# Kernel tuning notes

Measured on AMD Instinct MI355X. Metric: run time of the kernel, lower is better.

Reference implementation:

```python
import jax, jax.numpy as jnp
import numpy as np

B, TQ, TP, D = 4, 512, 512, 256


def setup_inputs() -> dict:
    key = jax.random.key(0)
    ks = jax.random.split(key, 5)
    return {
        "q": jax.random.normal(ks[0], (B, TQ, D), dtype=jnp.float32),
        "p": jax.random.normal(ks[1], (B, TP, D), dtype=jnp.float32),
        "W0": jax.random.normal(ks[2], (D, D), dtype=jnp.float32) / np.sqrt(D),
        "W1": jax.random.normal(ks[3], (D, D), dtype=jnp.float32) / np.sqrt(D),
        "vc": jax.random.normal(ks[4], (D, 1), dtype=jnp.float32) * 0.05,
    }


def reference(q, p, W0, W1, vc):
    # q: [B,Tq,Dq], p: [B,Tp,Dp]
    prod_q = jnp.einsum('bqd,de->bqe', q, W0)   # [B,Tq,dim]
    prod_p = jnp.einsum('bpd,de->bpe', p, W1)   # [B,Tp,dim]
    # additive attention energies: tanh over broadcast sum [B,Tp,Tq,dim]
    energy = jnp.tanh(prod_p[:, :, None, :] + prod_q[:, None, :, :])
    scores = jnp.einsum('bpqe,e->bpq', energy, vc[:, 0])  # [B,Tp,Tq]
    # original softmax is over axis=-2 of [B,Tp,Tq], i.e. the Tp axis
    weights = jax.nn.softmax(scores, axis=1)   # [B,Tp,Tq]
    # weighted sum over the Tq axis of (tiled) q
    attention_q = jnp.einsum('bpq,bqd->bpd', weights, q)  # [B,Tp,Dq]
    return attention_q
```

## Files before the change

kernel.cpp:

```cpp
#include <hip/hip_runtime.h>

#define NB 4
#define TT 512
#define DD 256
#define K2L2E    2.885390081777927f
#define NEG2L2E (-2.885390081777927f)

#if defined(__has_builtin)
# if __has_builtin(__builtin_amdgcn_global_load_lds)
#  define HAS_GLL 1
# endif
#endif

typedef float v2f __attribute__((ext_vector_type(2)));

__device__ __forceinline__ v2f pk_fma(v2f a, v2f b, v2f c) {
#if defined(__has_builtin)
# if __has_builtin(__builtin_elementwise_fma)
    return __builtin_elementwise_fma(a, b, c);
# else
    v2f r; r.x = __builtin_fmaf(a.x, b.x, c.x); r.y = __builtin_fmaf(a.y, b.y, c.y); return r;
# endif
#else
    v2f r; r.x = __builtin_fmaf(a.x, b.x, c.x); r.y = __builtin_fmaf(a.y, b.y, c.y); return r;
#endif
}
__device__ __forceinline__ v2f splat2(float s) { v2f r; r.x = s; r.y = s; return r; }

__device__ __forceinline__ void stage16(const float* __restrict__ g, float* l) {
#ifdef HAS_GLL
    __builtin_amdgcn_global_load_lds((const __attribute__((address_space(1))) void*)g,
                                     (__attribute__((address_space(3))) void*)l, 16, 0, 0);
#else
    *(float4*)l = *(const float4*)g;
#endif
}

__global__ __launch_bounds__(256) void proj_exp_kernel(
    const float* __restrict__ qin, const float* __restrict__ pin,
    const float* __restrict__ W0, const float* __restrict__ W1,
    float* __restrict__ expQ, float* __restrict__ expP)
{
    const int blk = blockIdx.x;
    const int wh = blk >> 8, tid = blk & 255;
    const int m0 = (tid >> 2) * 32, n0 = (tid & 3) * 64;
    const float* A = wh ? pin : qin;
    const float* W = wh ? W1 : W0;

    __shared__ __align__(16) float As[32 * 34];
    __shared__ __align__(16) float Bs[32 * 64];

    const int t  = threadIdx.x;
    const int ar = t >> 3, ac4 = (t & 7) * 4;
    const int br = t >> 4, bc4 = (t & 15) * 4;
    const int tm = wh ? (t >> 4) : (t & 15);
    const int tn = wh ? (t & 15) : (t >> 4);

    const float* Ap = A + (long)(m0 + ar) * DD + ac4;

    float4 av  = *(const float4*)Ap;
    float4 bv0 = *(const float4*)(W + (long)br * DD + n0 + bc4);
    float4 bv1 = *(const float4*)(W + (long)(br + 16) * DD + n0 + bc4);

    v2f accv[2][2];
    accv[0][0] = splat2(0.f); accv[0][1] = splat2(0.f);
    accv[1][0] = splat2(0.f); accv[1][1] = splat2(0.f);

    for (int c = 0; c < 8; ++c) {
        As[(ac4 + 0) * 34 + ar] = av.x;
        As[(ac4 + 1) * 34 + ar] = av.y;
        As[(ac4 + 2) * 34 + ar] = av.z;
        As[(ac4 + 3) * 34 + ar] = av.w;
        *(float4*)&Bs[br * 64 + bc4]        = bv0;
        *(float4*)&Bs[(br + 16) * 64 + bc4] = bv1;
        __syncthreads();
        if (c < 7) {
            int k1 = (c + 1) * 32;
            av  = *(const float4*)(Ap + k1);
            bv0 = *(const float4*)(W + (long)(k1 + br) * DD + n0 + bc4);
            bv1 = *(const float4*)(W + (long)(k1 + 16 + br) * DD + n0 + bc4);
        }
        #pragma unroll
        for (int kk = 0; kk < 32; ++kk) {
            float2 a = *(const float2*)&As[kk * 34 + 2 * tm];
            float4 b = *(const float4*)&Bs[kk * 64 + 4 * tn];
            v2f b01; b01.x = b.x; b01.y = b.y;
            v2f b23; b23.x = b.z; b23.y = b.w;
            accv[0][0] = pk_fma(splat2(a.x), b01, accv[0][0]);
            accv[0][1] = pk_fma(splat2(a.x), b23, accv[0][1]);
            accv[1][0] = pk_fma(splat2(a.y), b01, accv[1][0]);
            accv[1][1] = pk_fma(splat2(a.y), b23, accv[1][1]);
        }
        __syncthreads();
    }

    float acc[2][4];
    #pragma unroll
    for (int i = 0; i < 2; ++i) {
        acc[i][0] = accv[i][0].x; acc[i][1] = accv[i][0].y;
        acc[i][2] = accv[i][1].x; acc[i][3] = accv[i][1].y;
    }

    const int bi = m0 >> 9;
    const int ml = m0 & 511;
    if (wh) {
        #pragma unroll
        for (int i = 0; i < 2; ++i) {
            float4 st;
            st.x = __builtin_amdgcn_exp2f(acc[i][0] * K2L2E);
            st.y = __builtin_amdgcn_exp2f(acc[i][1] * K2L2E);
            st.z = __builtin_amdgcn_exp2f(acc[i][2] * K2L2E);
            st.w = __builtin_amdgcn_exp2f(acc[i][3] * K2L2E);
            *(float4*)(expP + ((long)bi * TT + ml + 2 * tm + i) * DD + n0 + 4 * tn) = st;
        }
    } else {
        #pragma unroll
        for (int j = 0; j < 4; ++j) {
            int d = n0 + 4 * tn + j;
            float2 st;
            st.x = __builtin_amdgcn_exp2f(acc[0][j] * K2L2E);
            st.y = __builtin_amdgcn_exp2f(acc[1][j] * K2L2E);
            *(float2*)(expQ + ((long)bi * DD + d) * TT + ml + 2 * tm) = st;
        }
    }
}

__global__ __launch_bounds__(512) void score_kernel(
    const float* __restrict__ expP, const float* __restrict__ expQ,
    const float* __restrict__ vc, float* __restrict__ ebuf, float* __restrict__ lpart)
{
    const int b = blockIdx.z, pt = blockIdx.y, qt = blockIdx.x;
    const int p0 = pt * 64, q0 = qt * 64;
    const int t  = threadIdx.x;
    const int h  = t >> 8;
    const int u  = t & 255;
    const int qx = u & 15;
    const int py = u >> 4;
    const int sw = py & 7;

    __shared__ __align__(16) float PA[64 * 256];
    __shared__ __align__(16) float QB[256 * 64];
    __shared__ __align__(16) float vcs[DD];

    const float* gP = expP + ((long)b * TT + p0) * DD;
    const float* gQ = expQ + (long)b * DD * TT + q0;

    #pragma unroll
    for (int s = 0; s < 8; ++s) {
        int f = t + 512 * s;
        int pr = f >> 6, j = f & 63;
        stage16(gP + (long)pr * DD + 4 * (j ^ ((pr >> 2) & 7)), &PA[f * 4]);
    }
    #pragma unroll
    for (int s = 0; s < 8; ++s) {
        int f = t + 512 * s;
        int d = f >> 4, o4 = (f & 15) * 4;
        stage16(gQ + (long)d * TT + o4, &QB[f * 4]);
    }
    if (t < DD) vcs[t] = vc[t];
    __syncthreads();

    v2f acc[4][2];
    #pragma unroll
    for (int i = 0; i < 4; ++i) { acc[i][0] = splat2(0.f); acc[i][1] = splat2(0.f); }
    const v2f one = splat2(1.0f);
    const float* vcb = &vcs[h * 128];

    #pragma unroll 4
    for (int dq = 0; dq < 32; ++dq) {
        const int dj = h * 32 + dq;
        float4 vq = *(const float4*)&vcb[4 * dq];
        const int sq = 4 * (dj ^ sw);
        float4 A0 = *(const float4*)&PA[(4 * py + 0) * 256 + sq];
        float4 A1 = *(const float4*)&PA[(4 * py + 1) * 256 + sq];
        float4 A2 = *(const float4*)&PA[(4 * py + 2) * 256 + sq];
        float4 A3 = *(const float4*)&PA[(4 * py + 3) * 256 + sq];
        const int db = (4 * dj) * 64 + 4 * qx;
        float4 B0 = *(const float4*)&QB[db];
        float4 B1 = *(const float4*)&QB[db + 64];
        float4 B2 = *(const float4*)&QB[db + 128];
        float4 B3 = *(const float4*)&QB[db + 192];
        v2f b0l; b0l.x = B0.x; b0l.y = B0.y;  v2f b0h; b0h.x = B0.z; b0h.y = B0.w;
        v2f b1l; b1l.x = B1.x; b1l.y = B1.y;  v2f b1h; b1h.x = B1.z; b1h.y = B1.w;
        v2f b2l; b2l.x = B2.x; b2l.y = B2.y;  v2f b2h; b2h.x = B2.z; b2h.y = B2.w;
        v2f b3l; b3l.x = B3.x; b3l.y = B3.y;  v2f b3h; b3h.x = B3.z; b3h.y = B3.w;
        #pragma unroll
        for (int i = 0; i < 4; ++i) {
            float4 a = (i == 0) ? A0 : (i == 1) ? A1 : (i == 2) ? A2 : A3;
            {
                v2f f0 = pk_fma(splat2(a.x), b0l, one);
                v2f f1 = pk_fma(splat2(a.y), b1l, one);
                v2f f2 = pk_fma(splat2(a.z), b2l, one);
                v2f f3 = pk_fma(splat2(a.w), b3l, one);
                v2f t01 = f0 * f1;
                v2f t23 = f2 * f3;
                v2f den = t01 * t23;
                v2f n01 = pk_fma(splat2(vq.x), f1, splat2(vq.y) * f0);
                v2f n23 = pk_fma(splat2(vq.z), f3, splat2(vq.w) * f2);
                v2f num = pk_fma(n01, t23, n23 * t01);
                v2f r;
                r.x = __builtin_amdgcn_rcpf(den.x);
                r.y = __builtin_amdgcn_rcpf(den.y);
                acc[i][0] = pk_fma(num, r, acc[i][0]);
            }
            {
                v2f f0 = pk_fma(splat2(a.x), b0h, one);
                v2f f1 = pk_fma(splat2(a.y), b1h, one);
                v2f f2 = pk_fma(splat2(a.z), b2h, one);
                v2f f3 = pk_fma(splat2(a.w), b3h, one);
                v2f t01 = f0 * f1;
                v2f t23 = f2 * f3;
                v2f den = t01 * t23;
                v2f n01 = pk_fma(splat2(vq.x), f1, splat2(vq.y) * f0);
                v2f n23 = pk_fma(splat2(vq.z), f3, splat2(vq.w) * f2);
                v2f num = pk_fma(n01, t23, n23 * t01);
                v2f r;
                r.x = __builtin_amdgcn_rcpf(den.x);
                r.y = __builtin_amdgcn_rcpf(den.y);
                acc[i][1] = pk_fma(num, r, acc[i][1]);
            }
        }
    }

    __syncthreads();
    float* scr = &PA[0];
    if (h == 1) {
        #pragma unroll
        for (int i = 0; i < 4; ++i) {
            float4 st;
            st.x = acc[i][0].x; st.y = acc[i][0].y;
            st.z = acc[i][1].x; st.w = acc[i][1].y;
            *(float4*)&scr[(4 * py + i) * 64 + 4 * qx] = st;
        }
    }
    __syncthreads();
    float* scr2 = &QB[0];
    if (h == 0) {
        float* eb = ebuf + ((long)b * TT + p0) * TT + q0;
        float4 colp; colp.x = 0.f; colp.y = 0.f; colp.z = 0.f; colp.w = 0.f;
        #pragma unroll
        for (int i = 0; i < 4; ++i) {
            float4 o = *(const float4*)&scr[(4 * py + i) * 64 + 4 * qx];
            float4 ev;
            ev.x = __builtin_amdgcn_exp2f((acc[i][0].x + o.x) * NEG2L2E);
            ev.y = __builtin_amdgcn_exp2f((acc[i][0].y + o.y) * NEG2L2E);
            ev.z = __builtin_amdgcn_exp2f((acc[i][1].x + o.z) * NEG2L2E);
            ev.w = __builtin_amdgcn_exp2f((acc[i][1].y + o.w) * NEG2L2E);
            *(float4*)(eb + (long)(4 * py + i) * TT + 4 * qx) = ev;
            colp.x += ev.x; colp.y += ev.y; colp.z += ev.z; colp.w += ev.w;
        }
        *(float4*)&scr2[py * 64 + 4 * qx] = colp;
    }
    __syncthreads();
    if (t < 64) {
        float s = 0.f;
        #pragma unroll
        for (int r = 0; r < 16; ++r) s += scr2[r * 64 + t];
        lpart[((long)b * 8 + pt) * TT + q0 + t] = s;
    }
}

__global__ __launch_bounds__(256) void out_kernel(
    const float* __restrict__ ebuf, const float* __restrict__ qin,
    const float* __restrict__ lpart, float* __restrict__ out)
{
    const int b = blockIdx.z, pt = blockIdx.y, dt = blockIdx.x;
    const int m0 = pt * 32, n0 = dt * 32;
    const int t    = threadIdx.x;
    const int wv   = t >> 6;
    const int lane = t & 63;
    const int pg   = lane >> 3;
    const int dg   = lane & 7;

    __shared__ __align__(16) float smem[4 * 32 * 36];
    __shared__ float linv[TT];
    float* As = smem;
    float* Bs = smem + 64 * 36;

    #pragma unroll
    for (int s = 0; s < 2; ++s) {
        int qq = t + 256 * s;
        float sum = 0.f;
        #pragma unroll
        for (int pb = 0; pb < 8; ++pb) sum += lpart[((long)b * 8 + pb) * TT + qq];
        linv[qq] = __builtin_amdgcn_rcpf(sum);
    }
    __syncthreads();

    const float* Ab = ebuf + ((long)b * TT + m0) * TT;
    const float* Bb = qin + (long)b * TT * DD + n0;

    const int ar = t >> 3, ak4 = (t & 7) * 4;

    v2f acc[4][2];
    #pragma unroll
    for (int i = 0; i < 4; ++i) { acc[i][0] = splat2(0.f); acc[i][1] = splat2(0.f); }

    for (int c = 0; c < 8; ++c) {
        const int k0 = c * 64;
        #pragma unroll
        for (int s = 0; s < 2; ++s) {
            int f = t + 256 * s, kr = f >> 3, d4 = (f & 7) * 4;
            stage16(Bb + (long)(k0 + kr) * DD + d4, &Bs[f * 4]);
        }
        #pragma unroll
        for (int s = 0; s < 2; ++s) {
            int kq = ak4 + 32 * s;
            float4 a = *(const float4*)(Ab + (long)ar * TT + k0 + kq);
            float4 lv = *(const float4*)&linv[k0 + kq];
            As[(kq + 0) * 36 + ar] = a.x * lv.x;
            As[(kq + 1) * 36 + ar] = a.y * lv.y;
            As[(kq + 2) * 36 + ar] = a.z * lv.z;
            As[(kq + 3) * 36 + ar] = a.w * lv.w;
        }
        __syncthreads();
        const int kb = 16 * wv;
        #pragma unroll
        for (int u = 0; u < 16; ++u) {
            int kk = kb + u;
            float4 a  = *(const float4*)&As[kk * 36 + 4 * pg];
            float4 bq = *(const float4*)&Bs[kk * 32 + 4 * dg];
            v2f b0; b0.x = bq.x; b0.y = bq.y;
            v2f b1; b1.x = bq.z; b1.y = bq.w;
            acc[0][0] = pk_fma(splat2(a.x), b0, acc[0][0]);
            acc[0][1] = pk_fma(splat2(a.x), b1, acc[0][1]);
            acc[1][0] = pk_fma(splat2(a.y), b0, acc[1][0]);
            acc[1][1] = pk_fma(splat2(a.y), b1, acc[1][1]);
            acc[2][0] = pk_fma(splat2(a.z), b0, acc[2][0]);
            acc[2][1] = pk_fma(splat2(a.z), b1, acc[2][1]);
            acc[3][0] = pk_fma(splat2(a.w), b0, acc[3][0]);
            acc[3][1] = pk_fma(splat2(a.w), b1, acc[3][1]);
        }
        __syncthreads();
    }

    float* scr = smem;
    #pragma unroll
    for (int i = 0; i < 4; ++i) {
        *(v2f*)&scr[wv * 1152 + (4 * pg + i) * 36 + 4 * dg]     = acc[i][0];
        *(v2f*)&scr[wv * 1152 + (4 * pg + i) * 36 + 4 * dg + 2] = acc[i][1];
    }
    __syncthreads();
    {
        int pr = t >> 3, d0 = (t & 7) * 4;
        float4 s0 = *(const float4*)&scr[0 * 1152 + pr * 36 + d0];
        float4 s1 = *(const float4*)&scr[1 * 1152 + pr * 36 + d0];
        float4 s2 = *(const float4*)&scr[2 * 1152 + pr * 36 + d0];
        float4 s3 = *(const float4*)&scr[3 * 1152 + pr * 36 + d0];
        float4 v;
        v.x = (s0.x + s1.x) + (s2.x + s3.x);
        v.y = (s0.y + s1.y) + (s2.y + s3.y);
        v.z = (s0.z + s1.z) + (s2.z + s3.z);
        v.w = (s0.w + s1.w) + (s2.w + s3.w);
        *(float4*)(out + ((long)b * TT + m0 + pr) * DD + n0 + d0) = v;
    }
}

extern "C" void kernel_launch(void* const* d_in, const int* in_sizes, int n_in,
                              void* d_out, int out_size, void* d_ws, size_t ws_size,
                              hipStream_t stream) {
    const float* q  = (const float*)d_in[0];
    const float* p  = (const float*)d_in[1];
    const float* W0 = (const float*)d_in[2];
    const float* W1 = (const float*)d_in[3];
    const float* vc = (const float*)d_in[4];
    float* out = (float*)d_out;

    float* ws    = (float*)d_ws;
    float* expQ  = ws;
    float* expP  = ws + 524288;
    float* ebuf  = ws + 1048576;
    float* lpart = ws + 2097152;

    proj_exp_kernel<<<dim3(512), 256, 0, stream>>>(q, p, W0, W1, expQ, expP);
    score_kernel<<<dim3(8, 8, NB), 512, 0, stream>>>(expP, expQ, vc, ebuf, lpart);
    out_kernel<<<dim3(8, 16, NB), 256, 0, stream>>>(ebuf, q, lpart, out);
}
```

Measured before the change: 117.2 us.

## Double-buffer LDS tiles in output GEMM kernel with register prefetch

Splits the output kernel's shared-memory tiles into two buffers. The next k-chunk of the normalized weight matrix and of q is staged while the current chunk is being multiplied, and the A-operand global loads are prefetched two chunks ahead into registers. This drops one barrier per iteration and hides global-load latency behind the FMA loop. The cost is more LDS per block, which may lower occupancy, plus higher register pressure. The kernel also relies on the epilogue scratch fitting exactly inside the doubled A buffer.

```diff
diff --git a/kernel.cpp b/kernel.cpp
--- a/kernel.cpp
+++ b/kernel.cpp
@@ -272,10 +272,9 @@
     const int pg   = lane >> 3;
     const int dg   = lane & 7;
 
-    __shared__ __align__(16) float smem[4 * 32 * 36];
+    __shared__ __align__(16) float As[2][64 * 36];
+    __shared__ __align__(16) float Bs[2][64 * 32];
     __shared__ float linv[TT];
-    float* As = smem;
-    float* Bs = smem + 64 * 36;
 
     #pragma unroll
     for (int s = 0; s < 2; ++s) {
@@ -291,35 +290,63 @@
     const float* Bb = qin + (long)b * TT * DD + n0;
 
     const int ar = t >> 3, ak4 = (t & 7) * 4;
+    const float* Arow = Ab + (long)ar * TT;
+    const int bkr = t >> 3, bd4 = (t & 7) * 4;
+
+    stage16(Bb + (long)bkr * DD + bd4,        &Bs[0][t * 4]);
+    stage16(Bb + (long)(bkr + 32) * DD + bd4, &Bs[0][1024 + t * 4]);
+    float4 av0 = *(const float4*)(Arow + ak4);
+    float4 av1 = *(const float4*)(Arow + ak4 + 32);
+    {
+        float4 l0 = *(const float4*)&linv[ak4];
+        float4 l1 = *(const float4*)&linv[ak4 + 32];
+        As[0][(ak4 + 0) * 36 + ar] = av0.x * l0.x;
+        As[0][(ak4 + 1) * 36 + ar] = av0.y * l0.y;
+        As[0][(ak4 + 2) * 36 + ar] = av0.z * l0.z;
+        As[0][(ak4 + 3) * 36 + ar] = av0.w * l0.w;
+        As[0][(ak4 + 32) * 36 + ar] = av1.x * l1.x;
+        As[0][(ak4 + 33) * 36 + ar] = av1.y * l1.y;
+        As[0][(ak4 + 34) * 36 + ar] = av1.z * l1.z;
+        As[0][(ak4 + 35) * 36 + ar] = av1.w * l1.w;
+    }
+    av0 = *(const float4*)(Arow + 64 + ak4);
+    av1 = *(const float4*)(Arow + 64 + ak4 + 32);
+    __syncthreads();
 
     v2f acc[4][2];
     #pragma unroll
     for (int i = 0; i < 4; ++i) { acc[i][0] = splat2(0.f); acc[i][1] = splat2(0.f); }
 
+    int buf = 0;
     for (int c = 0; c < 8; ++c) {
-        const int k0 = c * 64;
-        #pragma unroll
-        for (int s = 0; s < 2; ++s) {
-            int f = t + 256 * s, kr = f >> 3, d4 = (f & 7) * 4;
-            stage16(Bb + (long)(k0 + kr) * DD + d4, &Bs[f * 4]);
-        }
-        #pragma unroll
-        for (int s = 0; s < 2; ++s) {
-            int kq = ak4 + 32 * s;
-            float4 a = *(const float4*)(Ab + (long)ar * TT + k0 + kq);
-            float4 lv = *(const float4*)&linv[k0 + kq];
-            As[(kq + 0) * 36 + ar] = a.x * lv.x;
-            As[(kq + 1) * 36 + ar] = a.y * lv.y;
-            As[(kq + 2) * 36 + ar] = a.z * lv.z;
-            As[(kq + 3) * 36 + ar] = a.w * lv.w;
-        }
-        __syncthreads();
+        if (c < 7) {
+            const int k1 = (c + 1) * 64;
+            stage16(Bb + (long)(k1 + bkr) * DD + bd4,      &Bs[buf ^ 1][t * 4]);
+            stage16(Bb + (long)(k1 + 32 + bkr) * DD + bd4, &Bs[buf ^ 1][1024 + t * 4]);
+            float4 l0 = *(const float4*)&linv[k1 + ak4];
+            float4 l1 = *(const float4*)&linv[k1 + ak4 + 32];
+            As[buf ^ 1][(ak4 + 0) * 36 + ar] = av0.x * l0.x;
+            As[buf ^ 1][(ak4 + 1) * 36 + ar] = av0.y * l0.y;
+            As[buf ^ 1][(ak4 + 2) * 36 + ar] = av0.z * l0.z;
+            As[buf ^ 1][(ak4 + 3) * 36 + ar] = av0.w * l0.w;
+            As[buf ^ 1][(ak4 + 32) * 36 + ar] = av1.x * l1.x;
+            As[buf ^ 1][(ak4 + 33) * 36 + ar] = av1.y * l1.y;
+            As[buf ^ 1][(ak4 + 34) * 36 + ar] = av1.z * l1.z;
+            As[buf ^ 1][(ak4 + 35) * 36 + ar] = av1.w * l1.w;
+            if (c < 6) {
+                const int k2 = (c + 2) * 64;
+                av0 = *(const float4*)(Arow + k2 + ak4);
+                av1 = *(const float4*)(Arow + k2 + ak4 + 32);
+            }
+        }
+        const float* as = &As[buf][0];
+        const float* bs = &Bs[buf][0];
         const int kb = 16 * wv;
         #pragma unroll
         for (int u = 0; u < 16; ++u) {
             int kk = kb + u;
-            float4 a  = *(const float4*)&As[kk * 36 + 4 * pg];
-            float4 bq = *(const float4*)&Bs[kk * 32 + 4 * dg];
+            float4 a  = *(const float4*)&as[kk * 36 + 4 * pg];
+            float4 bq = *(const float4*)&bs[kk * 32 + 4 * dg];
             v2f b0; b0.x = bq.x; b0.y = bq.y;
             v2f b1; b1.x = bq.z; b1.y = bq.w;
             acc[0][0] = pk_fma(splat2(a.x), b0, acc[0][0]);
@@ -332,9 +359,10 @@
             acc[3][1] = pk_fma(splat2(a.w), b1, acc[3][1]);
         }
         __syncthreads();
-    }
-
-    float* scr = smem;
+        buf ^= 1;
+    }
+
+    float* scr = &As[0][0];
     #pragma unroll
     for (int i = 0; i < 4; ++i) {
         *(v2f*)&scr[wv * 1152 + (4 * pg + i) * 36 + 4 * dg]     = acc[i][0];
```

Measured after the change: 116.5 us. About the same (-0.6%).
